# Optimization experiments

Hardware: AMD Instinct MI355X
Metric: run time of the kernel (lower is better)

## Reference

```python
import jax, jax.numpy as jnp
import numpy as np

N_NODES = 50000


def _gcn_norm(edge_index, num_nodes):
    # Add self-loops, then symmetric normalization deg^-1/2 A_hat deg^-1/2
    loop = jnp.arange(num_nodes, dtype=edge_index.dtype)
    src = jnp.concatenate([edge_index[0], loop])  # source j
    dst = jnp.concatenate([edge_index[1], loop])  # target i
    ones = jnp.ones(dst.shape[0], dtype=jnp.float32)
    deg = jax.ops.segment_sum(ones, dst, num_segments=num_nodes)
    dinv = jnp.where(deg > 0, jax.lax.rsqrt(deg), 0.0)
    norm = dinv[src] * dinv[dst]  # [E + N]
    return src, dst, norm


def _gcn_layer(x, src, dst, norm, W, b, num_nodes):
    h = x @ W                              # [N, out]
    m = h[src] * norm[:, None]             # gather + scale, [E+N, out]
    out = jax.ops.segment_sum(m, dst, num_segments=num_nodes)  # scatter-add
    return out + b


def setup_inputs() -> dict:
    key = jax.random.key(0)
    ks = jax.random.split(key, 8)
    d = 128
    E = 800000
    x = jax.random.normal(ks[0], (N_NODES, d), dtype=jnp.float32)
    edge_index = jax.random.randint(ks[1], (2, E), 0, N_NODES, dtype=jnp.int64)
    s = 1.0 / np.sqrt(d)
    W0 = jax.random.normal(ks[2], (d, d), dtype=jnp.float32) * s
    W1 = jax.random.normal(ks[3], (d, d), dtype=jnp.float32) * s
    W2 = jax.random.normal(ks[4], (d, d), dtype=jnp.float32) * s
    b0 = jnp.zeros((d,), dtype=jnp.float32)
    b1 = jnp.zeros((d,), dtype=jnp.float32)
    b2 = jnp.zeros((d,), dtype=jnp.float32)
    return {"x": x, "edge_index": edge_index, "W0": W0, "b0": b0,
            "W1": W1, "b1": b1, "W2": W2, "b2": b2}


def reference(x, edge_index, W0, b0, W1, b1, W2, b2):
    src, dst, norm = _gcn_norm(edge_index, N_NODES)
    for W, b in ((W0, b0), (W1, b1), (W2, b2)):  # k = 3 layers
        x = _gcn_layer(x, src, dst, norm, W, b, N_NODES)
        x = jax.nn.relu(x)
    return x
```

## Files before the change

kernel.cpp:

```cpp
#include <hip/hip_runtime.h>
#include <hip/hip_fp16.h>

#define D 128
#define BIN_CH 8192
#define CAP 6144

typedef _Float16 f16x4 __attribute__((ext_vector_type(4)));
typedef float f32x4 __attribute__((ext_vector_type(4)));

__global__ __launch_bounds__(256) void k_init(const int* __restrict__ ei32,
        const float* __restrict__ W0, const float* __restrict__ W1,
        const float* __restrict__ W2, int* __restrict__ flag,
        int* __restrict__ bcur, __half* __restrict__ Wt) {
    if (blockIdx.x == 0) {
        __shared__ int nz;
        if (threadIdx.x == 0) nz = 0;
        __syncthreads();
        int c = 0;
        for (int i = threadIdx.x; i < 1024; i += blockDim.x) {
            if (ei32[2 * i + 1] != 0) c++;
        }
        atomicAdd(&nz, c);
        bcur[threadIdx.x] = threadIdx.x * CAP;
        __syncthreads();
        if (threadIdx.x == 0) *flag = (nz == 0) ? 1 : 0;
        return;
    }
    int bb = blockIdx.x - 1;
    int which = bb >> 4;
    const float* W = (which == 0) ? W0 : (which == 1) ? W1 : W2;
    __half* dst = Wt + (size_t)which * D * D;
    int tid = (bb & 15) * 256 + threadIdx.x;
    int c  = tid >> 5;
    int k4 = (tid & 31) * 4;
    float w0 = W[(k4 + 0) * D + c];
    float w1 = W[(k4 + 1) * D + c];
    float w2 = W[(k4 + 2) * D + c];
    float w3 = W[(k4 + 3) * D + c];
    union { __half2 h2[2]; uint2 u; } pk;
    pk.h2[0] = __floats2half2_rn(w0, w1);
    pk.h2[1] = __floats2half2_rn(w2, w3);
    *(uint2*)&dst[(size_t)c * D + k4] = pk.u;
}

__device__ __forceinline__ int e_src(const void* ei, int e, int is64, int E) {
    return is64 ? (int)((const long long*)ei)[e] : ((const int*)ei)[e];
}
__device__ __forceinline__ int e_dst(const void* ei, int e, int is64, int E) {
    return is64 ? (int)((const long long*)ei)[E + e] : ((const int*)ei)[E + e];
}

__global__ __launch_bounds__(256) void k_binning(const void* __restrict__ ei, int E,
        const int* __restrict__ flag, int* __restrict__ bcur, int2* __restrict__ ebuck) {
    __shared__ int lcnt[256];
    __shared__ int lbase[256];
    int is64 = *flag;
    int t = threadIdx.x;
    int e0 = blockIdx.x * BIN_CH;
    int e1 = min(e0 + BIN_CH, E);
    lcnt[t] = 0;
    __syncthreads();
    for (int e = e0 + t; e < e1; e += 256) {
        int d = e_dst(ei, e, is64, E);
        atomicAdd(&lcnt[d >> 8], 1);
    }
    __syncthreads();
    int c = lcnt[t];
    if (c > 0) lbase[t] = atomicAdd(&bcur[t], c);
    __syncthreads();
    lcnt[t] = 0;
    __syncthreads();
    for (int e = e0 + t; e < e1; e += 256) {
        int s = e_src(ei, e, is64, E);
        int d = e_dst(ei, e, is64, E);
        int b = d >> 8;
        int idx = atomicAdd(&lcnt[b], 1);
        ebuck[lbase[b] + idx] = make_int2(s, d);
    }
}

__global__ __launch_bounds__(256) void k_bucket_build(const int2* __restrict__ ebuck,
        const int* __restrict__ bcur, int* __restrict__ row_start,
        unsigned short* __restrict__ deg, float* __restrict__ dinv,
        int* __restrict__ esrc, int N) {
    __shared__ int lcnt[256];
    __shared__ int sc[256];
    __shared__ int lbase2[256];
    int b = blockIdx.x;
    int t = threadIdx.x;
    int lo = b * CAP;
    int hi = bcur[b];
    lcnt[t] = 0;
    __syncthreads();
    for (int j = lo + t; j < hi; j += 256) {
        atomicAdd(&lcnt[ebuck[j].y & 255], 1);
    }
    __syncthreads();
    int cntv = lcnt[t];
    sc[t] = cntv;
    __syncthreads();
#pragma unroll
    for (int d = 1; d < 256; d <<= 1) {
        int tv = (t >= d) ? sc[t - d] : 0;
        __syncthreads();
        sc[t] += tv;
        __syncthreads();
    }
    lbase2[t] = lo + sc[t] - cntv;
    int node = (b << 8) + t;
    if (node < N) {
        row_start[node] = lbase2[t];
        deg[node] = (unsigned short)cntv;
        dinv[node] = rsqrtf((float)(cntv + 1));
    }
    lcnt[t] = 0;
    __syncthreads();
    for (int j = lo + t; j < hi; j += 256) {
        int2 ed = ebuck[j];
        int c = ed.y & 255;
        int idx = atomicAdd(&lcnt[c], 1);
        esrc[lbase2[c] + idx] = ed.x;
    }
}

template<bool IN16>
__global__ __launch_bounds__(256) void k_gemm_mfma(const void* __restrict__ xin,
        const __half* __restrict__ Wt, const float* __restrict__ dinv,
        __half* __restrict__ h, int N) {
    __shared__ __align__(16) char Ab[128 * 256];
    __shared__ __align__(16) char Bb[128 * 256];
    int t = threadIdx.x;
    int br = blockIdx.x * 128;

#pragma unroll
    for (int i = 0; i < 8; ++i) {
        int byte = (i * 256 + t) * 16;
        int c = byte >> 8;
        uint4 v = *(const uint4*)((const char*)Wt + byte);
        *(uint4*)(Bb + (byte ^ ((c & 7) << 4))) = v;
    }
    if (IN16) {
        const char* xp = (const char*)xin;
#pragma unroll
        for (int i = 0; i < 8; ++i) {
            int byte = (i * 256 + t) * 16;
            int row = byte >> 8;
            int gr = br + row;
            uint4 v = make_uint4(0, 0, 0, 0);
            if (gr < N) v = *(const uint4*)(xp + (size_t)gr * 256 + (byte & 255));
            *(uint4*)(Ab + (byte ^ ((row & 7) << 4))) = v;
        }
    } else {
        const float* xp = (const float*)xin;
#pragma unroll
        for (int i = 0; i < 16; ++i) {
            int fid = i * 256 + t;
            int row = fid >> 5;
            int col4 = (fid & 31) * 4;
            int gr = br + row;
            float4 v = make_float4(0.f, 0.f, 0.f, 0.f);
            if (gr < N) v = *(const float4*)&xp[(size_t)gr * D + col4];
            union { __half2 h2[2]; uint2 u; } pk;
            pk.h2[0] = __floats2half2_rn(v.x, v.y);
            pk.h2[1] = __floats2half2_rn(v.z, v.w);
            int byte = row * 256 + col4 * 2;
            *(uint2*)(Ab + (byte ^ ((row & 7) << 4))) = pk.u;
        }
    }
    __syncthreads();

    int w = t >> 6;
    int l = t & 63;
    int lrow = l & 15;
    int g = l >> 4;
    f32x4 acc[2][8] = {};
    int arow0 = w * 32 + lrow;
    int arow1 = arow0 + 16;
#pragma unroll
    for (int ks = 0; ks < 8; ++ks) {
        int kb = ks * 32 + g * 8;
        f16x4 a0 = *(const f16x4*)(Ab + ((arow0 * 256 + kb) ^ ((arow0 & 7) << 4)));
        f16x4 a1 = *(const f16x4*)(Ab + ((arow1 * 256 + kb) ^ ((arow1 & 7) << 4)));
#pragma unroll
        for (int nj = 0; nj < 8; ++nj) {
            int bc = nj * 16 + lrow;
            f16x4 b = *(const f16x4*)(Bb + ((bc * 256 + kb) ^ ((bc & 7) << 4)));
            acc[0][nj] = __builtin_amdgcn_mfma_f32_16x16x16f16(a0, b, acc[0][nj], 0, 0, 0);
            acc[1][nj] = __builtin_amdgcn_mfma_f32_16x16x16f16(a1, b, acc[1][nj], 0, 0, 0);
        }
    }
#pragma unroll
    for (int mi = 0; mi < 2; ++mi) {
        int rbase = br + w * 32 + mi * 16 + g * 4;
#pragma unroll
        for (int r = 0; r < 4; ++r) {
            int gr = rbase + r;
            if (gr < N) {
                float sc = dinv[gr];
#pragma unroll
                for (int nj = 0; nj < 8; ++nj) {
                    h[(size_t)gr * D + nj * 16 + lrow] = __float2half(acc[mi][nj][r] * sc);
                }
            }
        }
    }
}

__device__ __forceinline__ void acc_row(uint4 u, float* a) {
    float2 q;
    q = __half22float2(*(const __half2*)&u.x); a[0] += q.x; a[1] += q.y;
    q = __half22float2(*(const __half2*)&u.y); a[2] += q.x; a[3] += q.y;
    q = __half22float2(*(const __half2*)&u.z); a[4] += q.x; a[5] += q.y;
    q = __half22float2(*(const __half2*)&u.w); a[6] += q.x; a[7] += q.y;
}

template<int WRITE_F32>
__global__ __launch_bounds__(256) void k_agg(const __half* __restrict__ h,
        const int* __restrict__ row_start, const unsigned short* __restrict__ deg,
        const int* __restrict__ esrc, const float* __restrict__ dinv,
        const float* __restrict__ bias, float* __restrict__ out,
        __half* __restrict__ act, int N) {
    int node = (blockIdx.x * blockDim.x + threadIdx.x) >> 4;
    int l16 = threadIdx.x & 15;
    if (node >= N) return;
    float di = dinv[node];
    const uint4* hv = (const uint4*)h;
    int j0 = row_start[node];
    int j1 = j0 + deg[node];

    float a[8] = {};
    acc_row(hv[(size_t)node * 16 + l16], a);

    int j = j0;
    for (; j + 8 <= j1; j += 8) {
        int s0 = esrc[j],     s1 = esrc[j + 1], s2 = esrc[j + 2], s3 = esrc[j + 3];
        int s4 = esrc[j + 4], s5 = esrc[j + 5], s6 = esrc[j + 6], s7 = esrc[j + 7];
        uint4 u0 = hv[(size_t)s0 * 16 + l16];
        uint4 u1 = hv[(size_t)s1 * 16 + l16];
        uint4 u2 = hv[(size_t)s2 * 16 + l16];
        uint4 u3 = hv[(size_t)s3 * 16 + l16];
        uint4 u4 = hv[(size_t)s4 * 16 + l16];
        uint4 u5 = hv[(size_t)s5 * 16 + l16];
        uint4 u6 = hv[(size_t)s6 * 16 + l16];
        uint4 u7 = hv[(size_t)s7 * 16 + l16];
        acc_row(u0, a); acc_row(u1, a); acc_row(u2, a); acc_row(u3, a);
        acc_row(u4, a); acc_row(u5, a); acc_row(u6, a); acc_row(u7, a);
    }
    for (; j + 4 <= j1; j += 4) {
        int s0 = esrc[j], s1 = esrc[j + 1], s2 = esrc[j + 2], s3 = esrc[j + 3];
        uint4 u0 = hv[(size_t)s0 * 16 + l16];
        uint4 u1 = hv[(size_t)s1 * 16 + l16];
        uint4 u2 = hv[(size_t)s2 * 16 + l16];
        uint4 u3 = hv[(size_t)s3 * 16 + l16];
        acc_row(u0, a); acc_row(u1, a); acc_row(u2, a); acc_row(u3, a);
    }
    for (; j < j1; ++j) {
        acc_row(hv[(size_t)esrc[j] * 16 + l16], a);
    }
    const float4* b4 = (const float4*)bias;
    float4 bv0 = b4[l16 * 2], bv1 = b4[l16 * 2 + 1];
    float o[8];
    o[0] = fmaxf(fmaf(a[0], di, bv0.x), 0.f);
    o[1] = fmaxf(fmaf(a[1], di, bv0.y), 0.f);
    o[2] = fmaxf(fmaf(a[2], di, bv0.z), 0.f);
    o[3] = fmaxf(fmaf(a[3], di, bv0.w), 0.f);
    o[4] = fmaxf(fmaf(a[4], di, bv1.x), 0.f);
    o[5] = fmaxf(fmaf(a[5], di, bv1.y), 0.f);
    o[6] = fmaxf(fmaf(a[6], di, bv1.z), 0.f);
    o[7] = fmaxf(fmaf(a[7], di, bv1.w), 0.f);
    if (WRITE_F32) {
        float4* o4 = (float4*)out;
        o4[(size_t)node * 32 + l16 * 2]     = make_float4(o[0], o[1], o[2], o[3]);
        o4[(size_t)node * 32 + l16 * 2 + 1] = make_float4(o[4], o[5], o[6], o[7]);
    } else {
        union { __half2 h2[4]; uint4 u; } pk;
        pk.h2[0] = __floats2half2_rn(o[0], o[1]);
        pk.h2[1] = __floats2half2_rn(o[2], o[3]);
        pk.h2[2] = __floats2half2_rn(o[4], o[5]);
        pk.h2[3] = __floats2half2_rn(o[6], o[7]);
        ((uint4*)act)[(size_t)node * 16 + l16] = pk.u;
    }
}

extern "C" void kernel_launch(void* const* d_in, const int* in_sizes, int n_in,
                              void* d_out, int out_size, void* d_ws, size_t ws_size,
                              hipStream_t stream) {
    const float* x  = (const float*)d_in[0];
    const void*  ei = d_in[1];
    const float* W0 = (const float*)d_in[2];
    const float* b0 = (const float*)d_in[3];
    const float* W1 = (const float*)d_in[4];
    const float* b1 = (const float*)d_in[5];
    const float* W2 = (const float*)d_in[6];
    const float* b2 = (const float*)d_in[7];
    float* out = (float*)d_out;

    const int N = in_sizes[0] / D;
    const int E = in_sizes[1] / 2;

    char* ws = (char*)d_ws;
    size_t off = 0;
    auto alloc = [&](size_t bytes) {
        char* p = ws + off;
        off = (off + bytes + 255) & ~(size_t)255;
        return p;
    };
    int*            flag      = (int*)alloc(4);
    int*            bcur      = (int*)alloc(256 * 4);
    int*            row_start = (int*)alloc((size_t)N * 4);
    unsigned short* deg       = (unsigned short*)alloc((size_t)N * 2);
    float*          dinv      = (float*)alloc((size_t)N * 4);
    int*            esrc      = (int*)alloc((size_t)256 * CAP * 4);
    __half*         hbuf      = (__half*)alloc((size_t)N * D * 2);
    __half*         act       = (__half*)alloc((size_t)N * D * 2);
    __half*         Wt        = (__half*)alloc((size_t)3 * D * D * 2);
    int2*           ebuck     = (int2*)hbuf;
    (void)ws_size;

    const int nbuck = (N + 255) >> 8;
    const int nbin  = (E + BIN_CH - 1) / BIN_CH;

    k_init<<<49, 256, 0, stream>>>((const int*)ei, W0, W1, W2, flag, bcur, Wt);
    k_binning<<<nbin, 256, 0, stream>>>(ei, E, flag, bcur, ebuck);
    k_bucket_build<<<nbuck, 256, 0, stream>>>(ebuck, bcur, row_start, deg, dinv, esrc, N);

    const int gemm_grid = (N + 127) / 128;
    const int agg_grid  = (N + 15) / 16;

    k_gemm_mfma<false><<<gemm_grid, 256, 0, stream>>>(x, Wt, dinv, hbuf, N);
    k_agg<0><<<agg_grid, 256, 0, stream>>>(hbuf, row_start, deg, esrc, dinv, b0, out, act, N);
    k_gemm_mfma<true><<<gemm_grid, 256, 0, stream>>>(act, Wt + (size_t)D * D, dinv, hbuf, N);
    k_agg<0><<<agg_grid, 256, 0, stream>>>(hbuf, row_start, deg, esrc, dinv, b1, out, act, N);
    k_gemm_mfma<true><<<gemm_grid, 256, 0, stream>>>(act, Wt + (size_t)2 * D * D, dinv, hbuf, N);
    k_agg<1><<<agg_grid, 256, 0, stream>>>(hbuf, row_start, deg, esrc, dinv, b2, out, act, N);
}
```

Baseline: 187.7 us.

## Split feature columns into XCD-affine chunks so each XCD's L2 holds one slice

Stores the intermediate h and activation buffers column-chunked: four chunks of 32 halves (64 B per node). The aggregation grid maps block IDs so each pair of XCDs only gathers from one chunk. The per-XCD gather working set drops from the full 12.8 MB h buffer to a 3.2 MB slice, which is meant to make the random neighbour gathers hit in L2. In exchange each gather is only 64 B per node, four threads per node instead of sixteen. The scheme also relies on round-robin block-to-XCD dispatch, and the GEMM stores become more scattered.

```diff
diff --git a/kernel.cpp b/kernel.cpp
--- a/kernel.cpp
+++ b/kernel.cpp
@@ -146,8 +146,12 @@
             int byte = (i * 256 + t) * 16;
             int row = byte >> 8;
             int gr = br + row;
+            int co = byte & 255;
             uint4 v = make_uint4(0, 0, 0, 0);
-            if (gr < N) v = *(const uint4*)(xp + (size_t)gr * 256 + (byte & 255));
+            if (gr < N) {
+                int chunk = co >> 6;
+                v = *(const uint4*)(xp + (size_t)chunk * N * 64 + (size_t)gr * 64 + (co & 63));
+            }
             *(uint4*)(Ab + (byte ^ ((row & 7) << 4))) = v;
         }
     } else {
@@ -199,7 +203,9 @@
                 float sc = dinv[gr];
 #pragma unroll
                 for (int nj = 0; nj < 8; ++nj) {
-                    h[(size_t)gr * D + nj * 16 + lrow] = __float2half(acc[mi][nj][r] * sc);
+                    size_t idx = (size_t)(nj >> 1) * N * 32 + (size_t)gr * 32
+                               + (nj & 1) * 16 + lrow;
+                    h[idx] = __float2half(acc[mi][nj][r] * sc);
                 }
             }
         }
@@ -220,45 +226,48 @@
         const int* __restrict__ esrc, const float* __restrict__ dinv,
         const float* __restrict__ bias, float* __restrict__ out,
         __half* __restrict__ act, int N) {
-    int node = (blockIdx.x * blockDim.x + threadIdx.x) >> 4;
-    int l16 = threadIdx.x & 15;
+    int xcd   = blockIdx.x & 7;
+    int chunk = xcd >> 1;
+    int rank  = ((blockIdx.x >> 3) << 1) + (xcd & 1);
+    int node = rank * 64 + (threadIdx.x >> 2);
+    int l4 = threadIdx.x & 3;
     if (node >= N) return;
     float di = dinv[node];
-    const uint4* hv = (const uint4*)h;
+    const uint4* hv = (const uint4*)(h + (size_t)chunk * N * 32);
     int j0 = row_start[node];
     int j1 = j0 + deg[node];
 
     float a[8] = {};
-    acc_row(hv[(size_t)node * 16 + l16], a);
+    acc_row(hv[(size_t)node * 4 + l4], a);
 
     int j = j0;
     for (; j + 8 <= j1; j += 8) {
         int s0 = esrc[j],     s1 = esrc[j + 1], s2 = esrc[j + 2], s3 = esrc[j + 3];
         int s4 = esrc[j + 4], s5 = esrc[j + 5], s6 = esrc[j + 6], s7 = esrc[j + 7];
-        uint4 u0 = hv[(size_t)s0 * 16 + l16];
-        uint4 u1 = hv[(size_t)s1 * 16 + l16];
-        uint4 u2 = hv[(size_t)s2 * 16 + l16];
-        uint4 u3 = hv[(size_t)s3 * 16 + l16];
-        uint4 u4 = hv[(size_t)s4 * 16 + l16];
-        uint4 u5 = hv[(size_t)s5 * 16 + l16];
-        uint4 u6 = hv[(size_t)s6 * 16 + l16];
-        uint4 u7 = hv[(size_t)s7 * 16 + l16];
+        uint4 u0 = hv[(size_t)s0 * 4 + l4];
+        uint4 u1 = hv[(size_t)s1 * 4 + l4];
+        uint4 u2 = hv[(size_t)s2 * 4 + l4];
+        uint4 u3 = hv[(size_t)s3 * 4 + l4];
+        uint4 u4 = hv[(size_t)s4 * 4 + l4];
+        uint4 u5 = hv[(size_t)s5 * 4 + l4];
+        uint4 u6 = hv[(size_t)s6 * 4 + l4];
+        uint4 u7 = hv[(size_t)s7 * 4 + l4];
         acc_row(u0, a); acc_row(u1, a); acc_row(u2, a); acc_row(u3, a);
         acc_row(u4, a); acc_row(u5, a); acc_row(u6, a); acc_row(u7, a);
     }
     for (; j + 4 <= j1; j += 4) {
         int s0 = esrc[j], s1 = esrc[j + 1], s2 = esrc[j + 2], s3 = esrc[j + 3];
-        uint4 u0 = hv[(size_t)s0 * 16 + l16];
-        uint4 u1 = hv[(size_t)s1 * 16 + l16];
-        uint4 u2 = hv[(size_t)s2 * 16 + l16];
-        uint4 u3 = hv[(size_t)s3 * 16 + l16];
+        uint4 u0 = hv[(size_t)s0 * 4 + l4];
+        uint4 u1 = hv[(size_t)s1 * 4 + l4];
+        uint4 u2 = hv[(size_t)s2 * 4 + l4];
+        uint4 u3 = hv[(size_t)s3 * 4 + l4];
         acc_row(u0, a); acc_row(u1, a); acc_row(u2, a); acc_row(u3, a);
     }
     for (; j < j1; ++j) {
-        acc_row(hv[(size_t)esrc[j] * 16 + l16], a);
+        acc_row(hv[(size_t)esrc[j] * 4 + l4], a);
     }
     const float4* b4 = (const float4*)bias;
-    float4 bv0 = b4[l16 * 2], bv1 = b4[l16 * 2 + 1];
+    float4 bv0 = b4[chunk * 8 + l4 * 2], bv1 = b4[chunk * 8 + l4 * 2 + 1];
     float o[8];
     o[0] = fmaxf(fmaf(a[0], di, bv0.x), 0.f);
     o[1] = fmaxf(fmaf(a[1], di, bv0.y), 0.f);
@@ -270,15 +279,15 @@
     o[7] = fmaxf(fmaf(a[7], di, bv1.w), 0.f);
     if (WRITE_F32) {
         float4* o4 = (float4*)out;
-        o4[(size_t)node * 32 + l16 * 2]     = make_float4(o[0], o[1], o[2], o[3]);
-        o4[(size_t)node * 32 + l16 * 2 + 1] = make_float4(o[4], o[5], o[6], o[7]);
+        o4[(size_t)node * 32 + chunk * 8 + l4 * 2]     = make_float4(o[0], o[1], o[2], o[3]);
+        o4[(size_t)node * 32 + chunk * 8 + l4 * 2 + 1] = make_float4(o[4], o[5], o[6], o[7]);
     } else {
         union { __half2 h2[4]; uint4 u; } pk;
         pk.h2[0] = __floats2half2_rn(o[0], o[1]);
         pk.h2[1] = __floats2half2_rn(o[2], o[3]);
         pk.h2[2] = __floats2half2_rn(o[4], o[5]);
         pk.h2[3] = __floats2half2_rn(o[6], o[7]);
-        ((uint4*)act)[(size_t)node * 16 + l16] = pk.u;
+        ((uint4*)act)[(size_t)chunk * N * 4 + (size_t)node * 4 + l4] = pk.u;
     }
 }
 
@@ -325,12 +334,13 @@
     k_bucket_build<<<nbuck, 256, 0, stream>>>(ebuck, bcur, row_start, deg, dinv, esrc, N);
 
     const int gemm_grid = (N + 127) / 128;
-    const int agg_grid  = (N + 15) / 16;
+    const int ranks     = (N + 63) / 64;
+    const int aggB      = (((ranks + 1) / 2)) * 8;
 
     k_gemm_mfma<false><<<gemm_grid, 256, 0, stream>>>(x, Wt, dinv, hbuf, N);
-    k_agg<0><<<agg_grid, 256, 0, stream>>>(hbuf, row_start, deg, esrc, dinv, b0, out, act, N);
+    k_agg<0><<<aggB, 256, 0, stream>>>(hbuf, row_start, deg, esrc, dinv, b0, out, act, N);
     k_gemm_mfma<true><<<gemm_grid, 256, 0, stream>>>(act, Wt + (size_t)D * D, dinv, hbuf, N);
-    k_agg<0><<<agg_grid, 256, 0, stream>>>(hbuf, row_start, deg, esrc, dinv, b1, out, act, N);
+    k_agg<0><<<aggB, 256, 0, stream>>>(hbuf, row_start, deg, esrc, dinv, b1, out, act, N);
     k_gemm_mfma<true><<<gemm_grid, 256, 0, stream>>>(act, Wt + (size_t)2 * D * D, dinv, hbuf, N);
-    k_agg<1><<<agg_grid, 256, 0, stream>>>(hbuf, row_start, deg, esrc, dinv, b2, out, act, N);
-}
+    k_agg<1><<<aggB, 256, 0, stream>>>(hbuf, row_start, deg, esrc, dinv, b2, out, act, N);
+}
```

Result: faster. 176.8 us (median of 2 runs) (-5.8%).
